# Performance work log

Hardware: AMD Instinct MI355X
Metric: run time of the kernel (lower is better)

## Reference

```python
import jax, jax.numpy as jnp
import numpy as np

MAX_DISP = 4  # matches init_kwargs


def setup_inputs() -> dict:
    key = jax.random.key(0)
    k1, k2 = jax.random.split(key)
    fmap1 = jax.random.normal(k1, (8, 256, 64, 128), dtype=jnp.float32)
    fmap2 = jax.random.normal(k2, (8, 256, 64, 128), dtype=jnp.float32)
    return {"fmap1": fmap1, "fmap2": fmap2}


def reference(fmap1, fmap2):
    # corr(x,y,dx,dy) = sum_c fmap1[c,y,x] * fmap2[c,y+dy,x+dx]
    pad = MAX_DISP
    B, C, H, W = fmap1.shape
    f2p = jnp.pad(fmap2, ((0, 0), (0, 0), (pad, pad), (pad, pad)))
    side = 2 * pad + 1  # 9 -> 81 displacements total
    # Loop over the small fixed set of 81 static displacements; each term is a
    # fused elementwise-multiply + channel reduction (einsum over c).
    corrs = [
        jnp.einsum('bchw,bchw->bhw', fmap1, f2p[:, :, y0:y0 + H, x0:x0 + W])
        for y0 in range(side)
        for x0 in range(side)
    ]
    return jnp.stack(corrs, axis=1)  # (B, 81, H, W)
```

## Files before the change

### kernel.cpp

```cpp
#include <hip/hip_runtime.h>


namespace {
constexpr int B_ = 8, C_ = 256, H_ = 64, W_ = 128;
constexpr int SIDE = 9, ND = 81, PAD = 4;
constexpr int HW = H_ * W_;
constexpr int CB = 32;
constexpr int HP = 72, WP = 144;
constexpr size_t NW2 = (size_t)B_ * CB * HP * WP;
constexpr size_t WS_BYTES = NW2 * 16;
constexpr int PERB = (int)(NW2 / B_);
}

typedef __attribute__((ext_vector_type(8))) short short8;
typedef __attribute__((ext_vector_type(4))) float float4v;

__device__ __forceinline__ unsigned bf16rne(float f) {
  unsigned u = __float_as_uint(f);
  return (u + 0x7fffu + ((u >> 16) & 1u)) >> 16;
}
__device__ __forceinline__ unsigned packbf2(float lo, float hi) {
  return bf16rne(lo) | (bf16rne(hi) << 16);
}

__global__ __launch_bounds__(256)
void cvt_f2(const float* __restrict__ f2, uint4* __restrict__ w2) {
  const int id = blockIdx.x;
  const int b = id & 7;
  const int e = (id >> 3) * 256 + threadIdx.x;
  const int xp = e % WP;
  const int r = e / WP;
  const int yp = r % HP;
  const int cb = r / HP;

  const int yg = yp - PAD, xg = xp - PAD;
  uint4 o = {0u, 0u, 0u, 0u};
  if (yg >= 0 && yg < H_ && xg >= 0 && xg < W_) {
    const float* s = f2 + ((size_t)(b * C_ + cb * 8) * H_ + yg) * W_ + xg;
    o.x = packbf2(s[0 * HW], s[1 * HW]);
    o.y = packbf2(s[2 * HW], s[3 * HW]);
    o.z = packbf2(s[4 * HW], s[5 * HW]);
    o.w = packbf2(s[6 * HW], s[7 * HW]);
  }
  w2[(size_t)b * PERB + e] = o;
}

__global__ __launch_bounds__(256, 4)
void corr_mfma(const float* __restrict__ f1, const uint4* __restrict__ w2,
               float* __restrict__ out) {
  const int id = blockIdx.x;
  const int b = id & 7;
  const int k = id >> 3;
  const int bx = k & 3;
  const int y = k >> 2;

  const int t = threadIdx.x;
  const int lane = t & 63;
  const int wv = t >> 6;
  const int jm = bx * 2 + (wv >> 1);
  const int half = wv & 1;
  const int v = lane & 15;
  const int q = lane >> 4;
  const int dyb = half * 5;
  const int ndy = 5 - half;

  float4v acc0[5], acc1[5];
#pragma unroll
  for (int i = 0; i < 5; ++i) {
    acc0[i] = (float4v){0.f, 0.f, 0.f, 0.f};
    acc1[i] = (float4v){0.f, 0.f, 0.f, 0.f};
  }

  const float* a_base =
      f1 + ((size_t)(b * C_ + q * 8) * H_ + y) * W_ + 16 * jm + v;
  const uint4* b_base =
      w2 + ((size_t)(b * CB + q) * HP + (y + dyb)) * WP + 16 * jm + v;

#pragma unroll
  for (int ch = 0; ch < 8; ++ch) {
    uint4 Bv[10];
    const uint4* bc = b_base + (size_t)(ch * 4) * (HP * WP);
#pragma unroll
    for (int i = 0; i < 5; ++i) {
      if (i < ndy) {
        Bv[2 * i] = bc[(size_t)i * WP];
        Bv[2 * i + 1] = bc[(size_t)i * WP + 16];
      }
    }
    float av[8];
#pragma unroll
    for (int j = 0; j < 8; ++j) av[j] = a_base[(size_t)(ch * 32 + j) * HW];
    uint4 afu;
    afu.x = packbf2(av[0], av[1]);
    afu.y = packbf2(av[2], av[3]);
    afu.z = packbf2(av[4], av[5]);
    afu.w = packbf2(av[6], av[7]);
    const short8 af = __builtin_bit_cast(short8, afu);

#pragma unroll
    for (int i = 0; i < 5; ++i) {
      if (i < ndy) {
        acc0[i] = __builtin_amdgcn_mfma_f32_16x16x32_bf16(
            af, __builtin_bit_cast(short8, Bv[2 * i]), acc0[i], 0, 0, 0);
        acc1[i] = __builtin_amdgcn_mfma_f32_16x16x32_bf16(
            af, __builtin_bit_cast(short8, Bv[2 * i + 1]), acc1[i], 0, 0, 0);
      }
    }
  }

#pragma unroll
  for (int i = 0; i < 5; ++i) {
    if (i < ndy) {
      const int dy = dyb + i;
#pragma unroll
      for (int r = 0; r < 4; ++r) {
        const int m = q * 4 + r;
        const int x = 16 * jm + m;
        const int dx0 = v - m;
        if (dx0 >= 0 && dx0 <= 8)
          out[(((size_t)b * ND + dy * SIDE + dx0) * H_ + y) * W_ + x] = acc0[i][r];
        const int dx1 = v - m + 16;
        if (dx1 <= 8)
          out[(((size_t)b * ND + dy * SIDE + dx1) * H_ + y) * W_ + x] = acc1[i][r];
      }
    }
  }
}

namespace fb {
constexpr int PXS = 20, F2PX = 80, F1PX = 64, KC = 32, NCH = C_ / KC;
constexpr int F2U = SIDE * (F2PX / 4) * (KC / 2);
constexpr int F1U = (F1PX / 4) * (KC / 2);
constexpr int NU = F2U + F1U;
}

__global__ __launch_bounds__(512, 4)
void corr_fallback(const float* __restrict__ f1, const float* __restrict__ f2,
                   float* __restrict__ out) {
  using namespace fb;
  __shared__ __align__(16) unsigned f2s[SIDE * F2PX * PXS];
  __shared__ __align__(16) unsigned f1s[F1PX * PXS];

  const int t = threadIdx.x;
  const int bx = blockIdx.x, by = blockIdx.y, b = blockIdx.z;
  const int x0B = bx * 64;
  const int lane = t & 63, wv = t >> 6;
  const int wt = wv >> 1, half = wv & 1;
  const int dyb = half * 5, ndy = 5 - half;
  const int v = lane & 15, q = lane >> 4;

  float4v acc0[5], acc1[5];
#pragma unroll
  for (int i = 0; i < 5; ++i) {
    acc0[i] = (float4v){0.f, 0.f, 0.f, 0.f};
    acc1[i] = (float4v){0.f, 0.f, 0.f, 0.f};
  }
  const float* __restrict__ f1b = f1 + (size_t)b * C_ * HW;
  const float* __restrict__ f2b = f2 + (size_t)b * C_ * HW;

  for (int ch = 0; ch < NCH; ++ch) {
    const int c0 = ch * KC;
    if (ch) __syncthreads();
    for (int u = t; u < NU; u += 512) {
      if (u < F2U) {
        const int cp = u & 15;
        const int rp = u >> 4;
        const int pxq = rp % 20;
        const int r = rp / 20;
        const int yg = by + r - PAD;
        const int xb = x0B - PAD + pxq * 4;
        float4 va = make_float4(0.f, 0.f, 0.f, 0.f), vb = va;
        if (yg >= 0 && yg < H_ && xb >= 0 && xb <= W_ - 4) {
          const float* p = f2b + ((size_t)(c0 + 2 * cp) * H_ + yg) * W_ + xb;
          va = *(const float4*)p;
          vb = *(const float4*)(p + HW);
        }
        unsigned* d = &f2s[(r * F2PX + pxq * 4) * PXS + cp];
        d[0 * PXS] = packbf2(va.x, vb.x);
        d[1 * PXS] = packbf2(va.y, vb.y);
        d[2 * PXS] = packbf2(va.z, vb.z);
        d[3 * PXS] = packbf2(va.w, vb.w);
      } else {
        const int u2 = u - F2U;
        const int cp = u2 & 15;
        const int pxq = u2 >> 4;
        const float* p = f1b + ((size_t)(c0 + 2 * cp) * H_ + by) * W_ + x0B + pxq * 4;
        const float4 va = *(const float4*)p;
        const float4 vb = *(const float4*)(p + HW);
        unsigned* d = &f1s[(pxq * 4) * PXS + cp];
        d[0 * PXS] = packbf2(va.x, vb.x);
        d[1 * PXS] = packbf2(va.y, vb.y);
        d[2 * PXS] = packbf2(va.z, vb.z);
        d[3 * PXS] = packbf2(va.w, vb.w);
      }
    }
    __syncthreads();

    const short8 af =
        __builtin_bit_cast(short8, *(const uint4*)&f1s[(16 * wt + v) * PXS + 4 * q]);
#pragma unroll
    for (int i = 0; i < 5; ++i) {
      if (i < ndy) {
        const int dy = dyb + i;
        const unsigned* fbp = &f2s[(dy * F2PX + 16 * wt + v) * PXS + 4 * q];
        const short8 b0 = __builtin_bit_cast(short8, *(const uint4*)fbp);
        const short8 b1 = __builtin_bit_cast(short8, *(const uint4*)(fbp + 16 * PXS));
        acc0[i] = __builtin_amdgcn_mfma_f32_16x16x32_bf16(af, b0, acc0[i], 0, 0, 0);
        acc1[i] = __builtin_amdgcn_mfma_f32_16x16x32_bf16(af, b1, acc1[i], 0, 0, 0);
      }
    }
  }
#pragma unroll
  for (int i = 0; i < 5; ++i) {
    if (i < ndy) {
      const int dy = dyb + i;
#pragma unroll
      for (int r = 0; r < 4; ++r) {
        const int m = q * 4 + r;
        const int x = x0B + 16 * wt + m;
        const int dx0 = v - m;
        if (dx0 >= 0 && dx0 <= 8)
          out[(((size_t)b * ND + dy * SIDE + dx0) * H_ + by) * W_ + x] = acc0[i][r];
        const int dx1 = v - m + 16;
        if (dx1 <= 8)
          out[(((size_t)b * ND + dy * SIDE + dx1) * H_ + by) * W_ + x] = acc1[i][r];
      }
    }
  }
}

extern "C" void kernel_launch(void* const* d_in, const int* in_sizes, int n_in,
                              void* d_out, int out_size, void* d_ws, size_t ws_size,
                              hipStream_t stream) {
  const float* f1 = (const float*)d_in[0];
  const float* f2 = (const float*)d_in[1];
  float* out = (float*)d_out;

  if (ws_size >= WS_BYTES) {
    uint4* w2 = (uint4*)d_ws;
    cvt_f2<<<dim3((int)(NW2 / 256)), 256, 0, stream>>>(f2, w2);
    corr_mfma<<<dim3(2048), 256, 0, stream>>>(f1, w2, out);
  } else {
    corr_fallback<<<dim3(2, H_, B_), 512, 0, stream>>>(f1, f2, out);
  }
}
```

Before: 217.1 us.

## Fuse bf16 conversion into single LDS-tiled correlation kernel with 2D tiles

Removes the separate pass that converts fmap2 to padded bf16 in workspace, as well as the fallback path, and replaces them with one fused kernel. Each block stages an 8-row by 16-column tile of fmap1 and a 16x32 haloed tile of fmap2 in shared memory per 32-channel chunk, converting to bf16 on the fly. Each wave computes all 9 dy rows for one output row. This removes the workspace write and re-read and reuses fmap2 halo rows across 8 output rows, but the grid is only 512 blocks and each wave holds more accumulators.

```diff
diff --git a/kernel.cpp b/kernel.cpp
--- a/kernel.cpp
+++ b/kernel.cpp
@@ -5,11 +5,15 @@
 constexpr int B_ = 8, C_ = 256, H_ = 64, W_ = 128;
 constexpr int SIDE = 9, ND = 81, PAD = 4;
 constexpr int HW = H_ * W_;
-constexpr int CB = 32;
-constexpr int HP = 72, WP = 144;
-constexpr size_t NW2 = (size_t)B_ * CB * HP * WP;
-constexpr size_t WS_BYTES = NW2 * 16;
-constexpr int PERB = (int)(NW2 / B_);
+constexpr int KC = 32;
+constexpr int NCH = C_ / KC;
+constexpr int YB = 8;
+constexpr int RWS = YB + 2 * PAD;
+constexpr int XB = 16;
+constexpr int F2PX = 32;
+constexpr int PXS = KC / 2 + 4;
+constexpr int F2U = RWS * (F2PX / 4) * (KC / 2);
+constexpr int F1U = YB * (XB / 4) * (KC / 2);
 }
 
 typedef __attribute__((ext_vector_type(8))) short short8;
@@ -23,224 +27,116 @@
   return bf16rne(lo) | (bf16rne(hi) << 16);
 }
 
-__global__ __launch_bounds__(256)
-void cvt_f2(const float* __restrict__ f2, uint4* __restrict__ w2) {
-  const int id = blockIdx.x;
-  const int b = id & 7;
-  const int e = (id >> 3) * 256 + threadIdx.x;
-  const int xp = e % WP;
-  const int r = e / WP;
-  const int yp = r % HP;
-  const int cb = r / HP;
+__global__ __launch_bounds__(512, 4)
+void corr_fused(const float* __restrict__ f1, const float* __restrict__ f2,
+                float* __restrict__ out) {
+  __shared__ __align__(16) unsigned f2s[RWS * F2PX * PXS];
+  __shared__ __align__(16) unsigned f1s[YB * XB * PXS];
 
-  const int yg = yp - PAD, xg = xp - PAD;
-  uint4 o = {0u, 0u, 0u, 0u};
-  if (yg >= 0 && yg < H_ && xg >= 0 && xg < W_) {
-    const float* s = f2 + ((size_t)(b * C_ + cb * 8) * H_ + yg) * W_ + xg;
-    o.x = packbf2(s[0 * HW], s[1 * HW]);
-    o.y = packbf2(s[2 * HW], s[3 * HW]);
-    o.z = packbf2(s[4 * HW], s[5 * HW]);
-    o.w = packbf2(s[6 * HW], s[7 * HW]);
-  }
-  w2[(size_t)b * PERB + e] = o;
-}
-
-__global__ __launch_bounds__(256, 4)
-void corr_mfma(const float* __restrict__ f1, const uint4* __restrict__ w2,
-               float* __restrict__ out) {
   const int id = blockIdx.x;
   const int b = id & 7;
   const int k = id >> 3;
-  const int bx = k & 3;
-  const int y = k >> 2;
+  const int xg = k & 7;
+  const int yg = k >> 3;
+  const int x0 = xg * XB;
+  const int y0 = yg * YB;
 
   const int t = threadIdx.x;
   const int lane = t & 63;
-  const int wv = t >> 6;
-  const int jm = bx * 2 + (wv >> 1);
-  const int half = wv & 1;
+  const int w = t >> 6;
   const int v = lane & 15;
   const int q = lane >> 4;
-  const int dyb = half * 5;
-  const int ndy = 5 - half;
 
-  float4v acc0[5], acc1[5];
+  float4v acc[SIDE][2];
 #pragma unroll
-  for (int i = 0; i < 5; ++i) {
-    acc0[i] = (float4v){0.f, 0.f, 0.f, 0.f};
-    acc1[i] = (float4v){0.f, 0.f, 0.f, 0.f};
+  for (int i = 0; i < SIDE; ++i) {
+    acc[i][0] = (float4v){0.f, 0.f, 0.f, 0.f};
+    acc[i][1] = (float4v){0.f, 0.f, 0.f, 0.f};
   }
 
-  const float* a_base =
-      f1 + ((size_t)(b * C_ + q * 8) * H_ + y) * W_ + 16 * jm + v;
-  const uint4* b_base =
-      w2 + ((size_t)(b * CB + q) * HP + (y + dyb)) * WP + 16 * jm + v;
-
-#pragma unroll
-  for (int ch = 0; ch < 8; ++ch) {
-    uint4 Bv[10];
-    const uint4* bc = b_base + (size_t)(ch * 4) * (HP * WP);
-#pragma unroll
-    for (int i = 0; i < 5; ++i) {
-      if (i < ndy) {
-        Bv[2 * i] = bc[(size_t)i * WP];
-        Bv[2 * i + 1] = bc[(size_t)i * WP + 16];
-      }
-    }
-    float av[8];
-#pragma unroll
-    for (int j = 0; j < 8; ++j) av[j] = a_base[(size_t)(ch * 32 + j) * HW];
-    uint4 afu;
-    afu.x = packbf2(av[0], av[1]);
-    afu.y = packbf2(av[2], av[3]);
-    afu.z = packbf2(av[4], av[5]);
-    afu.w = packbf2(av[6], av[7]);
-    const short8 af = __builtin_bit_cast(short8, afu);
-
-#pragma unroll
-    for (int i = 0; i < 5; ++i) {
-      if (i < ndy) {
-        acc0[i] = __builtin_amdgcn_mfma_f32_16x16x32_bf16(
-            af, __builtin_bit_cast(short8, Bv[2 * i]), acc0[i], 0, 0, 0);
-        acc1[i] = __builtin_amdgcn_mfma_f32_16x16x32_bf16(
-            af, __builtin_bit_cast(short8, Bv[2 * i + 1]), acc1[i], 0, 0, 0);
-      }
-    }
-  }
-
-#pragma unroll
-  for (int i = 0; i < 5; ++i) {
-    if (i < ndy) {
-      const int dy = dyb + i;
-#pragma unroll
-      for (int r = 0; r < 4; ++r) {
-        const int m = q * 4 + r;
-        const int x = 16 * jm + m;
-        const int dx0 = v - m;
-        if (dx0 >= 0 && dx0 <= 8)
-          out[(((size_t)b * ND + dy * SIDE + dx0) * H_ + y) * W_ + x] = acc0[i][r];
-        const int dx1 = v - m + 16;
-        if (dx1 <= 8)
-          out[(((size_t)b * ND + dy * SIDE + dx1) * H_ + y) * W_ + x] = acc1[i][r];
-      }
-    }
-  }
-}
-
-namespace fb {
-constexpr int PXS = 20, F2PX = 80, F1PX = 64, KC = 32, NCH = C_ / KC;
-constexpr int F2U = SIDE * (F2PX / 4) * (KC / 2);
-constexpr int F1U = (F1PX / 4) * (KC / 2);
-constexpr int NU = F2U + F1U;
-}
-
-__global__ __launch_bounds__(512, 4)
-void corr_fallback(const float* __restrict__ f1, const float* __restrict__ f2,
-                   float* __restrict__ out) {
-  using namespace fb;
-  __shared__ __align__(16) unsigned f2s[SIDE * F2PX * PXS];
-  __shared__ __align__(16) unsigned f1s[F1PX * PXS];
-
-  const int t = threadIdx.x;
-  const int bx = blockIdx.x, by = blockIdx.y, b = blockIdx.z;
-  const int x0B = bx * 64;
-  const int lane = t & 63, wv = t >> 6;
-  const int wt = wv >> 1, half = wv & 1;
-  const int dyb = half * 5, ndy = 5 - half;
-  const int v = lane & 15, q = lane >> 4;
-
-  float4v acc0[5], acc1[5];
-#pragma unroll
-  for (int i = 0; i < 5; ++i) {
-    acc0[i] = (float4v){0.f, 0.f, 0.f, 0.f};
-    acc1[i] = (float4v){0.f, 0.f, 0.f, 0.f};
-  }
   const float* __restrict__ f1b = f1 + (size_t)b * C_ * HW;
   const float* __restrict__ f2b = f2 + (size_t)b * C_ * HW;
 
   for (int ch = 0; ch < NCH; ++ch) {
     const int c0 = ch * KC;
     if (ch) __syncthreads();
-    for (int u = t; u < NU; u += 512) {
-      if (u < F2U) {
-        const int cp = u & 15;
-        const int rp = u >> 4;
-        const int pxq = rp % 20;
-        const int r = rp / 20;
-        const int yg = by + r - PAD;
-        const int xb = x0B - PAD + pxq * 4;
-        float4 va = make_float4(0.f, 0.f, 0.f, 0.f), vb = va;
-        if (yg >= 0 && yg < H_ && xb >= 0 && xb <= W_ - 4) {
-          const float* p = f2b + ((size_t)(c0 + 2 * cp) * H_ + yg) * W_ + xb;
-          va = *(const float4*)p;
-          vb = *(const float4*)(p + HW);
-        }
-        unsigned* d = &f2s[(r * F2PX + pxq * 4) * PXS + cp];
-        d[0 * PXS] = packbf2(va.x, vb.x);
-        d[1 * PXS] = packbf2(va.y, vb.y);
-        d[2 * PXS] = packbf2(va.z, vb.z);
-        d[3 * PXS] = packbf2(va.w, vb.w);
-      } else {
-        const int u2 = u - F2U;
-        const int cp = u2 & 15;
-        const int pxq = u2 >> 4;
-        const float* p = f1b + ((size_t)(c0 + 2 * cp) * H_ + by) * W_ + x0B + pxq * 4;
-        const float4 va = *(const float4*)p;
-        const float4 vb = *(const float4*)(p + HW);
-        unsigned* d = &f1s[(pxq * 4) * PXS + cp];
-        d[0 * PXS] = packbf2(va.x, vb.x);
-        d[1 * PXS] = packbf2(va.y, vb.y);
-        d[2 * PXS] = packbf2(va.z, vb.z);
-        d[3 * PXS] = packbf2(va.w, vb.w);
+
+#pragma unroll
+    for (int u0 = 0; u0 < F2U; u0 += 512) {
+      const int u = u0 + t;
+      const int cp = u & 15;
+      const int t2 = u >> 4;
+      const int pxq = t2 & 7;
+      const int r = t2 >> 3;
+      const int ygl = y0 - PAD + r;
+      const int xb = x0 - PAD + pxq * 4;
+      float4 va = make_float4(0.f, 0.f, 0.f, 0.f), vb = va;
+      if (ygl >= 0 && ygl < H_ && xb >= 0 && xb <= W_ - 4) {
+        const float* p = f2b + ((size_t)(c0 + 2 * cp) * H_ + ygl) * W_ + xb;
+        va = *(const float4*)p;
+        vb = *(const float4*)(p + HW);
       }
+      unsigned* d = &f2s[(r * F2PX + pxq * 4) * PXS + cp];
+      d[0 * PXS] = packbf2(va.x, vb.x);
+      d[1 * PXS] = packbf2(va.y, vb.y);
+      d[2 * PXS] = packbf2(va.z, vb.z);
+      d[3 * PXS] = packbf2(va.w, vb.w);
+    }
+    {
+      const int cp = t & 15;
+      const int t2 = t >> 4;
+      const int pxq = t2 & 3;
+      const int r = t2 >> 2;
+      const float* p =
+          f1b + ((size_t)(c0 + 2 * cp) * H_ + (y0 + r)) * W_ + x0 + pxq * 4;
+      const float4 va = *(const float4*)p;
+      const float4 vb = *(const float4*)(p + HW);
+      unsigned* d = &f1s[(r * XB + pxq * 4) * PXS + cp];
+      d[0 * PXS] = packbf2(va.x, vb.x);
+      d[1 * PXS] = packbf2(va.y, vb.y);
+      d[2 * PXS] = packbf2(va.z, vb.z);
+      d[3 * PXS] = packbf2(va.w, vb.w);
     }
     __syncthreads();
 
-    const short8 af =
-        __builtin_bit_cast(short8, *(const uint4*)&f1s[(16 * wt + v) * PXS + 4 * q]);
+    const short8 af = __builtin_bit_cast(
+        short8, *(const uint4*)&f1s[(w * XB + v) * PXS + 4 * q]);
 #pragma unroll
-    for (int i = 0; i < 5; ++i) {
-      if (i < ndy) {
-        const int dy = dyb + i;
-        const unsigned* fbp = &f2s[(dy * F2PX + 16 * wt + v) * PXS + 4 * q];
-        const short8 b0 = __builtin_bit_cast(short8, *(const uint4*)fbp);
-        const short8 b1 = __builtin_bit_cast(short8, *(const uint4*)(fbp + 16 * PXS));
-        acc0[i] = __builtin_amdgcn_mfma_f32_16x16x32_bf16(af, b0, acc0[i], 0, 0, 0);
-        acc1[i] = __builtin_amdgcn_mfma_f32_16x16x32_bf16(af, b1, acc1[i], 0, 0, 0);
-      }
+    for (int dy = 0; dy < SIDE; ++dy) {
+      const unsigned* fp = &f2s[((w + dy) * F2PX + v) * PXS + 4 * q];
+      const short8 b0 = __builtin_bit_cast(short8, *(const uint4*)fp);
+      const short8 b1 =
+          __builtin_bit_cast(short8, *(const uint4*)(fp + 16 * PXS));
+      acc[dy][0] =
+          __builtin_amdgcn_mfma_f32_16x16x32_bf16(af, b0, acc[dy][0], 0, 0, 0);
+      acc[dy][1] =
+          __builtin_amdgcn_mfma_f32_16x16x32_bf16(af, b1, acc[dy][1], 0, 0, 0);
     }
   }
+
+  const int y = y0 + w;
+  float* outb = out + (size_t)b * ND * HW + (size_t)y * W_ + x0;
 #pragma unroll
-  for (int i = 0; i < 5; ++i) {
-    if (i < ndy) {
-      const int dy = dyb + i;
+  for (int dy = 0; dy < SIDE; ++dy) {
 #pragma unroll
-      for (int r = 0; r < 4; ++r) {
-        const int m = q * 4 + r;
-        const int x = x0B + 16 * wt + m;
-        const int dx0 = v - m;
-        if (dx0 >= 0 && dx0 <= 8)
-          out[(((size_t)b * ND + dy * SIDE + dx0) * H_ + by) * W_ + x] = acc0[i][r];
-        const int dx1 = v - m + 16;
-        if (dx1 <= 8)
-          out[(((size_t)b * ND + dy * SIDE + dx1) * H_ + by) * W_ + x] = acc1[i][r];
-      }
+    for (int r = 0; r < 4; ++r) {
+      const int m = q * 4 + r;
+      const int dx0 = v - m;
+      if (dx0 >= 0 && dx0 <= 8)
+        outb[(size_t)(dy * SIDE + dx0) * HW + m] = acc[dy][0][r];
+      const int dx1 = v - m + 16;
+      if (dx1 <= 8)
+        outb[(size_t)(dy * SIDE + dx1) * HW + m] = acc[dy][1][r];
     }
   }
 }
 
 extern "C" void kernel_launch(void* const* d_in, const int* in_sizes, int n_in,
-                              void* d_out, int out_size, void* d_ws, size_t ws_size,
-                              hipStream_t stream) {
+                              void* d_out, int out_size, void* d_ws,
+                              size_t ws_size, hipStream_t stream) {
+  (void)in_sizes; (void)n_in; (void)out_size; (void)d_ws; (void)ws_size;
   const float* f1 = (const float*)d_in[0];
   const float* f2 = (const float*)d_in[1];
   float* out = (float*)d_out;
-
-  if (ws_size >= WS_BYTES) {
-    uint4* w2 = (uint4*)d_ws;
-    cvt_f2<<<dim3((int)(NW2 / 256)), 256, 0, stream>>>(f2, w2);
-    corr_mfma<<<dim3(2048), 256, 0, stream>>>(f1, w2, out);
-  } else {
-    corr_fallback<<<dim3(2, H_, B_), 512, 0, stream>>>(f1, f2, out);
-  }
+  corr_fused<<<dim3(512), 512, 0, stream>>>(f1, f2, out);
 }
```

Result: faster. 178.8 us (-17.6%).
